# Optimization experiments

Hardware: AMD Instinct MI355X
Metric: run time of the kernel (lower is better)

Reference implementation:

```python
import jax, jax.numpy as jnp
import numpy as np

DIM = 1024; DEPTH = 2; HEADS = 8; DH = DIM // HEADS  # 128
BUCKET = 64; NHASH = 4; MULT = 4
B = 2; T = 4096
NBUCKETS = T // BUCKET  # 64
SCALE = DH ** -0.5
SELF_ATTN_VAL = -5e4  # TOKEN_SELF_ATTN_VALUE in reformer-pytorch
EPS = 1e-5


def layer_norm(x, g, b):
    m = jnp.mean(x, -1, keepdims=True)
    v = jnp.var(x, -1, keepdims=True)
    return (x - m) * jax.lax.rsqrt(v + EPS) * g + b


def lsh_attn(xn, Wqk, Wv, Wo, bo, rot):
    # xn: [B,T,DIM] already layer-normed. Shared-QK LSH attention (reformer-pytorch).
    qk = (xn @ Wqk).reshape(B, T, HEADS, DH).transpose(0, 2, 1, 3).reshape(B * HEADS, T, DH)
    v = (xn @ Wv).reshape(B, T, HEADS, DH).transpose(0, 2, 1, 3).reshape(B * HEADS, T, DH)
    bh = B * HEADS
    # --- hashing with random rotations ---
    rotated = jnp.einsum('btf,fhi->bhti', qk, rot)            # [bh,NHASH,T,NBUCKETS//2]
    rotated = jnp.concatenate([rotated, -rotated], -1)        # [bh,NHASH,T,NBUCKETS]
    buckets = jnp.argmax(rotated, -1)                         # [bh,NHASH,T]
    offs = (jnp.arange(NHASH) * NBUCKETS)[:, None]
    buckets = (buckets + offs).reshape(bh, NHASH * T)
    ticker = jnp.arange(NHASH * T)
    bt = buckets * T + (ticker % T)                           # unique keys -> stable-equivalent sort
    sticker = jnp.argsort(bt, axis=-1)                        # [bh, NHASH*T]
    undo = jnp.argsort(sticker, axis=-1)
    st = sticker % T                                          # original positions, bucket-sorted
    sqk = jnp.take_along_axis(qk, st[..., None], axis=1)
    sv = jnp.take_along_axis(v, st[..., None], axis=1)
    nchunks = NHASH * NBUCKETS
    bq_t = st.reshape(bh, nchunks, BUCKET)
    bqk = sqk.reshape(bh, nchunks, BUCKET, DH)
    bv = sv.reshape(bh, nchunks, BUCKET, DH)
    bq = bqk
    bk = bqk / jnp.clip(jnp.linalg.norm(bqk, axis=-1, keepdims=True), 1e-12)
    def look_one_back(a):
        extra = jnp.concatenate([a[:, -1:], a[:, :-1]], axis=1)
        return jnp.concatenate([a, extra], axis=2)
    bk = look_one_back(bk); bv = look_one_back(bv); bkv_t = look_one_back(bq_t)
    dots = jnp.einsum('bcie,bcje->bcij', bq, bk) * SCALE      # [bh,nchunks,BUCKET,2*BUCKET]
    self_mask = bq_t[..., :, None] == bkv_t[..., None, :]     # shared-QK: penalize i==j
    dots = jnp.where(self_mask, SELF_ATTN_VAL, dots)
    lse = jax.nn.logsumexp(dots, axis=-1, keepdims=True)
    p = jnp.exp(dots - lse)
    bo_ = jnp.einsum('bcij,bcje->bcie', p, bv)
    so = bo_.reshape(bh, NHASH * T, DH)
    slog = lse.reshape(bh, NHASH * T)
    o = jnp.take_along_axis(so, undo[..., None], axis=1)
    logits = jnp.take_along_axis(slog, undo, axis=1)
    o = o.reshape(bh, NHASH, T, DH)
    logits = logits.reshape(bh, NHASH, T, 1)
    probs = jnp.exp(logits - jax.nn.logsumexp(logits, axis=1, keepdims=True))
    out = jnp.sum(o * probs, axis=1)                          # combine hash rounds
    out = out.reshape(B, HEADS, T, DH).transpose(0, 2, 1, 3).reshape(B, T, HEADS * DH)
    return out @ Wo + bo


def setup_inputs() -> dict:
    key = jax.random.key(0)
    ks = jax.random.split(key, 16)
    s = 0.02
    d = {
        'x': jax.random.normal(ks[0], (B, T, DIM), jnp.float32),
        'ln1_g': jnp.ones((DEPTH, DIM), jnp.float32),
        'ln1_b': jnp.zeros((DEPTH, DIM), jnp.float32),
        'Wqk': jax.random.normal(ks[1], (DEPTH, DIM, HEADS * DH), jnp.float32) * s,
        'Wv': jax.random.normal(ks[2], (DEPTH, DIM, HEADS * DH), jnp.float32) * s,
        'Wo': jax.random.normal(ks[3], (DEPTH, HEADS * DH, DIM), jnp.float32) * s,
        'bo': jnp.zeros((DEPTH, DIM), jnp.float32),
        'ln2_g': jnp.ones((DEPTH, DIM), jnp.float32),
        'ln2_b': jnp.zeros((DEPTH, DIM), jnp.float32),
        'W1': jax.random.normal(ks[4], (DEPTH, DIM, DIM * MULT), jnp.float32) * s,
        'b1': jnp.zeros((DEPTH, DIM * MULT), jnp.float32),
        'W2': jax.random.normal(ks[5], (DEPTH, DIM * MULT, DIM), jnp.float32) * s,
        'b2': jnp.zeros((DEPTH, DIM), jnp.float32),
        'rotations': jax.random.normal(ks[6], (DEPTH, DH, NHASH, NBUCKETS // 2), jnp.float32),
    }
    return d


def reference(x, ln1_g, ln1_b, Wqk, Wv, Wo, bo, ln2_g, ln2_b, W1, b1, W2, b2, rotations):
    xx = jnp.concatenate([x, x], -1)  # [B,T,2*DIM] reversible pair
    def step(carry, p):
        g1, be1, wqk, wv, wo, bov, g2, be2, w1, bb1, w2, bb2, rot = p
        x1, x2 = jnp.split(carry, 2, axis=-1)
        y1 = x1 + lsh_attn(layer_norm(x2, g1, be1), wqk, wv, wo, bov, rot)
        h = layer_norm(y1, g2, be2)
        ff = jax.nn.gelu(h @ w1 + bb1, approximate=False) @ w2 + bb2
        y2 = x2 + ff
        return jnp.concatenate([y1, y2], -1), None
    params = (ln1_g, ln1_b, Wqk, Wv, Wo, bo, ln2_g, ln2_b, W1, b1, W2, b2, rotations)
    out, _ = jax.lax.scan(step, xx, params)
    y1, y2 = jnp.split(out, 2, axis=-1)
    return y1 + y2
```

## Files before the change

kernel.cpp:

```cpp
#include <hip/hip_runtime.h>
#include <hip/hip_bf16.h>
#include <cmath>

using bf16 = __hip_bfloat16;
typedef __attribute__((ext_vector_type(8))) short short8;
typedef __attribute__((ext_vector_type(4))) float floatx4;

__device__ __forceinline__ float bu2f(ushort u) { return __uint_as_float((unsigned)u << 16); }
__device__ __forceinline__ ushort f2bu(float f) {
  union { bf16 b; ushort u; } cv; cv.b = __float2bfloat16(f); return cv.u;
}
__device__ __forceinline__ void gl_lds16(const ushort* g, ushort* l) {
  __builtin_amdgcn_global_load_lds((const __attribute__((address_space(1))) unsigned*)g,
                                   (__attribute__((address_space(3))) unsigned*)l, 16, 0, 0);
}
__device__ __forceinline__ float fast_gelu(float x) {
  float z = 0.7978845608028654f * (x + 0.044715f * x * x * x);
  z = fmaxf(fminf(z, 10.f), -10.f);
  float e = __expf(2.f * z);
  float t = (e - 1.f) / (e + 1.f);
  return 0.5f * x * (1.f + t);
}

static constexpr int kT   = 4096;
static constexpr int kDim = 1024;
static constexpr float kScale   = 0.08838834764831845f;
static constexpr float kSelfVal = -5.0e4f;

__device__ __forceinline__ int sane_v(float f) { float a = fabsf(f); return (a > 1e-4f && a < 1e4f) ? 1 : 0; }

__global__ __launch_bounds__(256) void k_detect(const unsigned* __restrict__ x, int* __restrict__ flag) {
  __shared__ int cnt;
  int tid = threadIdx.x;
  if (tid == 0) cnt = 0;
  __syncthreads();
  int my = 0;
  const uint4* p = (const uint4*)x;
  for (int q = 0; q < 16; q++) {
    uint4 u = p[tid * 16 + q];
    my += sane_v(__uint_as_float(u.x << 16)) + sane_v(__uint_as_float(u.x & 0xffff0000u));
    my += sane_v(__uint_as_float(u.y << 16)) + sane_v(__uint_as_float(u.y & 0xffff0000u));
    my += sane_v(__uint_as_float(u.z << 16)) + sane_v(__uint_as_float(u.z & 0xffff0000u));
    my += sane_v(__uint_as_float(u.w << 16)) + sane_v(__uint_as_float(u.w & 0xffff0000u));
  }
  atomicAdd(&cnt, my);
  __syncthreads();
  if (tid == 0) flag[0] = (cnt >= 24576) ? 1 : 0;
}

__global__ __launch_bounds__(256) void k_cvt(const int* __restrict__ flag, const void* __restrict__ src,
                                             ushort* __restrict__ dst, int n) {
  int i = blockIdx.x * 256 + threadIdx.x;
  if (i >= n) return;
  dst[i] = (*flag) ? ((const ushort*)src)[i] : f2bu(((const float*)src)[i]);
}

__global__ __launch_bounds__(256) void k_init_any(const int* __restrict__ flag, const void* __restrict__ x,
                                                  float* __restrict__ x1, float* __restrict__ x2) {
  int i = blockIdx.x * 1024 + threadIdx.x * 4;
  float4 f;
  if (*flag) {
    ushort4 u = *(const ushort4*)((const ushort*)x + i);
    f.x = bu2f(u.x); f.y = bu2f(u.y); f.z = bu2f(u.z); f.w = bu2f(u.w);
  } else {
    f = *(const float4*)((const float*)x + i);
  }
  *(float4*)(x1 + i) = f;
  *(float4*)(x2 + i) = f;
}

__global__ __launch_bounds__(256) void k_final_any(const int* __restrict__ flag, const float* __restrict__ x1,
                                                   const float* __restrict__ x2, void* __restrict__ out) {
  int i = blockIdx.x * 1024 + threadIdx.x * 4;
  float4 a = *(const float4*)(x1 + i);
  float4 b = *(const float4*)(x2 + i);
  float4 s; s.x = a.x + b.x; s.y = a.y + b.y; s.z = a.z + b.z; s.w = a.w + b.w;
  if (*flag) {
    ushort4 u; u.x = f2bu(s.x); u.y = f2bu(s.y); u.z = f2bu(s.z); u.w = f2bu(s.w);
    *(ushort4*)((ushort*)out + i) = u;
  } else {
    *(float4*)((float*)out + i) = s;
  }
}

__global__ __launch_bounds__(256) void k_ln(const float* __restrict__ x, const ushort* __restrict__ g,
                                            const ushort* __restrict__ be, ushort* __restrict__ out) {
  __shared__ float ws[4], ws2[4];
  int row = blockIdx.x, tid = threadIdx.x;
  const float* xr = x + (size_t)row * kDim + tid * 4;
  float4 v = *(const float4*)xr;
  float s  = v.x + v.y + v.z + v.w;
  float s2 = v.x*v.x + v.y*v.y + v.z*v.z + v.w*v.w;
  #pragma unroll
  for (int off = 32; off; off >>= 1) { s += __shfl_down(s, off); s2 += __shfl_down(s2, off); }
  int wave = tid >> 6, lane = tid & 63;
  if (lane == 0) { ws[wave] = s; ws2[wave] = s2; }
  __syncthreads();
  s  = ws[0] + ws[1] + ws[2] + ws[3];
  s2 = ws2[0] + ws2[1] + ws2[2] + ws2[3];
  float mean = s * (1.f/1024.f);
  float var  = fmaxf(s2 * (1.f/1024.f) - mean*mean, 0.f);
  float rstd = rsqrtf(var + 1e-5f);
  int cb = tid * 4;
  ushort* o = out + (size_t)row * kDim + cb;
  o[0] = f2bu((v.x - mean) * rstd * bu2f(g[cb+0]) + bu2f(be[cb+0]));
  o[1] = f2bu((v.y - mean) * rstd * bu2f(g[cb+1]) + bu2f(be[cb+1]));
  o[2] = f2bu((v.z - mean) * rstd * bu2f(g[cb+2]) + bu2f(be[cb+2]));
  o[3] = f2bu((v.w - mean) * rstd * bu2f(g[cb+3]) + bu2f(be[cb+3]));
}

__global__ __launch_bounds__(256) void k_transpose2(const int* __restrict__ flag, const void* __restrict__ src_bf,
                                                    const void* __restrict__ src_f, ushort* __restrict__ out,
                                                    int K, int N) {
  __shared__ ushort tile[32][33];
  int isbf = *flag;
  int nb = blockIdx.x * 32, kb = blockIdx.y * 32;
  int tx = threadIdx.x & 31, ty = threadIdx.x >> 5;
  for (int r = ty; r < 32; r += 8) {
    size_t idx = (size_t)(kb + r) * N + nb + tx;
    tile[r][tx] = isbf ? ((const ushort*)src_bf)[idx] : f2bu(((const float*)src_f)[idx]);
  }
  __syncthreads();
  for (int r = ty; r < 32; r += 8) out[(size_t)(nb + r) * K + kb + tx] = tile[tx][r];
}

__global__ __launch_bounds__(256) void k_rot_t(const ushort* __restrict__ rot, ushort* __restrict__ rotT) {
  int tid = threadIdx.x;
  for (int idx = tid; idx < 16384; idx += 256) {
    int n = idx >> 7, k = idx & 127;
    rotT[idx] = rot[k * 128 + n];
  }
}

__global__ __launch_bounds__(256) void k_gemm(const ushort* __restrict__ A, const ushort* __restrict__ Bt,
                                              const ushort* __restrict__ bias, float* __restrict__ Cf,
                                              ushort* __restrict__ Cb, ushort* __restrict__ Cb2,
                                              int M, int N, int K, int mode) {
  __shared__ alignas(16) ushort As[128*64];
  __shared__ alignas(16) ushort Bs[128*64];
  const int tid = threadIdx.x;
  const int lane = tid & 63, wave = tid >> 6;
  const int m0 = blockIdx.y * 128, n0 = blockIdx.x * 128;
  const int wm = (wave & 1) * 64, wn = (wave >> 1) * 64;
  const int lr = lane & 15, lk = (lane >> 4) * 8;
  const int r8  = tid >> 3;
  const int cst = ((tid & 7) * 8) ^ ((r8 & 7) * 8);
  const int swz = (lr & 7) * 8;

  floatx4 acc[4][4];
  #pragma unroll
  for (int mi = 0; mi < 4; mi++)
    #pragma unroll
    for (int ni = 0; ni < 4; ni++) acc[mi][ni] = (floatx4){0.f, 0.f, 0.f, 0.f};

  const ushort* Ap = A  + (size_t)(m0 + r8) * K + cst;
  const ushort* Bp = Bt + (size_t)(n0 + r8) * K + cst;
  const size_t rstep = (size_t)32 * K;

  for (int k0 = 0; k0 < K; k0 += 64) {
    __syncthreads();
    #pragma unroll
    for (int i = 0; i < 4; i++) {
      gl_lds16(Ap + i * rstep + k0, As + i*2048 + wave*512);
      gl_lds16(Bp + i * rstep + k0, Bs + i*2048 + wave*512);
    }
    __syncthreads();
    #pragma unroll
    for (int ks = 0; ks < 2; ks++) {
      const int col = (ks*32 + lk) ^ swz;
      short8 a[4], b[4];
      #pragma unroll
      for (int mi = 0; mi < 4; mi++) a[mi] = *(const short8*)&As[(wm + mi*16 + lr)*64 + col];
      #pragma unroll
      for (int ni = 0; ni < 4; ni++) b[ni] = *(const short8*)&Bs[(wn + ni*16 + lr)*64 + col];
      #pragma unroll
      for (int mi = 0; mi < 4; mi++)
        #pragma unroll
        for (int ni = 0; ni < 4; ni++)
          acc[mi][ni] = __builtin_amdgcn_mfma_f32_16x16x32_bf16(a[mi], b[ni], acc[mi][ni], 0, 0, 0);
    }
  }
  #pragma unroll
  for (int mi = 0; mi < 4; mi++) {
    #pragma unroll
    for (int ni = 0; ni < 4; ni++) {
      int col = n0 + wn + ni*16 + lr;
      float bv = (mode == 1 || mode == 2) ? bu2f(bias[col]) : 0.f;
      #pragma unroll
      for (int q = 0; q < 4; q++) {
        int r2 = m0 + wm + mi*16 + (lane >> 4)*4 + q;
        float val = acc[mi][ni][q];
        if (mode == 0) {
          Cf[(size_t)r2 * N + col] = val;
        } else if (mode == 1) {
          Cf[(size_t)r2 * N + col] += val + bv;
        } else if (mode == 2) {
          Cb[(size_t)r2 * N + col] = f2bu(fast_gelu(val + bv));
        } else if (mode == 3) {
          Cb[(size_t)r2 * N + col] = f2bu(val);
        } else {
          ushort h = f2bu(val);
          Cb [(size_t)r2 * N + col] = h;
          Cb2[(size_t)r2 * N + col] = f2bu(val - bu2f(h));
        }
      }
    }
  }
}

__global__ __launch_bounds__(256) void k_bucket_mfma(const ushort* __restrict__ qkh, const ushort* __restrict__ qkl,
                                                     const ushort* __restrict__ rotT, int* __restrict__ bkt) {
  __shared__ alignas(16) ushort Bs[128*128];
  __shared__ alignas(16) ushort Ah[64*128];
  __shared__ alignas(16) ushort Al[64*128];
  const int tid = threadIdx.x;
  const int lane = tid & 63, wave = tid >> 6;
  const int lr = lane & 15, lk = (lane >> 4) * 8;
  const int tt = blockIdx.x * 64;
  const int bh = blockIdx.y;
  const int b = bh >> 3, hh = bh & 7;

  {
    int r = tid >> 2, c0 = (tid & 3) * 32;
    size_t base = ((size_t)(b * kT + tt + r)) * kDim + hh * 128 + c0;
    const uint4* sh = (const uint4*)(qkh + base);
    const uint4* sl = (const uint4*)(qkl + base);
    uint4* dh = (uint4*)&Ah[r * 128 + c0];
    uint4* dl = (uint4*)&Al[r * 128 + c0];
    #pragma unroll
    for (int i = 0; i < 4; i++) { dh[i] = sh[i]; dl[i] = sl[i]; }
  }
  {
    const uint4* src = (const uint4*)rotT;
    uint4* dst = (uint4*)Bs;
    for (int i = tid; i < 2048; i += 256) dst[i] = src[i];
  }
  __syncthreads();

  floatx4 acc[4][2];
  #pragma unroll
  for (int mi = 0; mi < 4; mi++) { acc[mi][0] = (floatx4){0,0,0,0}; acc[mi][1] = (floatx4){0,0,0,0}; }
  #pragma unroll
  for (int ks = 0; ks < 4; ks++) {
    short8 a[4], bb[2];
    #pragma unroll
    for (int ni = 0; ni < 2; ni++) bb[ni] = *(const short8*)&Bs[(wave*32 + ni*16 + lr)*128 + ks*32 + lk];
    #pragma unroll
    for (int mi = 0; mi < 4; mi++) a[mi] = *(const short8*)&Ah[(mi*16 + lr)*128 + ks*32 + lk];
    #pragma unroll
    for (int mi = 0; mi < 4; mi++)
      #pragma unroll
      for (int ni = 0; ni < 2; ni++)
        acc[mi][ni] = __builtin_amdgcn_mfma_f32_16x16x32_bf16(a[mi], bb[ni], acc[mi][ni], 0, 0, 0);
  }
  #pragma unroll
  for (int ks = 0; ks < 4; ks++) {
    short8 a[4], bb[2];
    #pragma unroll
    for (int ni = 0; ni < 2; ni++) bb[ni] = *(const short8*)&Bs[(wave*32 + ni*16 + lr)*128 + ks*32 + lk];
    #pragma unroll
    for (int mi = 0; mi < 4; mi++) a[mi] = *(const short8*)&Al[(mi*16 + lr)*128 + ks*32 + lk];
    #pragma unroll
    for (int mi = 0; mi < 4; mi++)
      #pragma unroll
      for (int ni = 0; ni < 2; ni++)
        acc[mi][ni] = __builtin_amdgcn_mfma_f32_16x16x32_bf16(a[mi], bb[ni], acc[mi][ni], 0, 0, 0);
  }

  #pragma unroll
  for (int mi = 0; mi < 4; mi++) {
    #pragma unroll
    for (int q = 0; q < 4; q++) {
      float v0 = acc[mi][0][q];
      float v1 = acc[mi][1][q];
      float best = v0; int bidx = lr;
      if (v1  > best) { best = v1;  bidx = 16 + lr; }
      if (-v0 > best) { best = -v0; bidx = 32 + lr; }
      if (-v1 > best) { best = -v1; bidx = 48 + lr; }
      #pragma unroll
      for (int m = 1; m <= 8; m <<= 1) {
        float ov = __shfl_xor(best, m);
        int   oi = __shfl_xor(bidx, m);
        if (ov > best || (ov == best && oi < bidx)) { best = ov; bidx = oi; }
      }
      if (lr == 0) {
        int row = mi*16 + ((lane >> 4) & 3)*4 + q;
        bkt[(bh*4 + wave)*4096 + tt + row] = bidx;
      }
    }
  }
}

__global__ __launch_bounds__(256) void k_sort(const int* __restrict__ bkt, int* __restrict__ st) {
  __shared__ unsigned char  hist[64*256];
  __shared__ unsigned short offs[64*256];
  __shared__ int base[64];
  int tid = threadIdx.x, grp = blockIdx.x;
  const int* bk = bkt + grp * 4096;
  for (int i = tid; i < 64*256; i += 256) hist[i] = 0;
  __syncthreads();
  int myb[16];
  #pragma unroll
  for (int j = 0; j < 16; j++) {
    myb[j] = bk[tid*16 + j];
    hist[myb[j]*256 + tid] += 1;
  }
  __syncthreads();
  if (tid < 64) {
    int run = 0;
    for (int t = 0; t < 256; t++) { offs[tid*256 + t] = (unsigned short)run; run += hist[tid*256 + t]; }
    base[tid] = run;
  }
  __syncthreads();
  if (tid == 0) {
    int run = 0;
    for (int b2 = 0; b2 < 64; b2++) { int c = base[b2]; base[b2] = run; run += c; }
  }
  __syncthreads();
  #pragma unroll
  for (int j = 0; j < 16; j++) {
    int b2 = myb[j];
    int r = 0;
    for (int jj = 0; jj < j; jj++) r += (myb[jj] == b2) ? 1 : 0;
    st[grp*4096 + base[b2] + (int)offs[b2*256 + tid] + r] = tid*16 + j;
  }
}

__global__ __launch_bounds__(256) void k_attn(const ushort* __restrict__ qkh, const ushort* __restrict__ vbuf,
                                              const int* __restrict__ st, ushort* __restrict__ o_r,
                                              float* __restrict__ lse_r) {
  __shared__ alignas(16) ushort KV[128*136];
  __shared__ alignas(16) ushort Ps[64*136];
  __shared__ float rnorm[128];
  __shared__ int   kposs[128];
  __shared__ float red1[64*4];
  __shared__ float red2[64*4];
  __shared__ float lrow[64];

  const int tid = threadIdx.x;
  const int bid = blockIdx.x;
  const int bh = bid >> 8;
  const int c  = bid & 255;
  const int h  = c >> 6;
  const int cprev = (c + 255) & 255;
  const int b  = bh >> 3, hh = bh & 7;
  const int lane = tid & 63, wave = tid >> 6;
  const int lr = lane & 15, lk = (lane >> 4) * 8;

  {
    int j = tid >> 1, half = tid & 1;
    int slot = (j < 64) ? (c*64 + j) : (cprev*64 + (j - 64));
    int pos = st[bh*16384 + slot];
    if (half == 0) kposs[j] = pos;
    const ushort* src = qkh + ((size_t)(b * kT + pos)) * kDim + hh*128 + half*64;
    float ss = 0.f;
    #pragma unroll
    for (int i2 = 0; i2 < 64; i2 += 8) {
      uint4 u = *(const uint4*)(src + i2);
      *(uint4*)&KV[j*136 + half*64 + i2] = u;
      float f0 = bu2f((ushort)(u.x & 0xffffu)), f1 = bu2f((ushort)(u.x >> 16));
      float f2 = bu2f((ushort)(u.y & 0xffffu)), f3 = bu2f((ushort)(u.y >> 16));
      float f4 = bu2f((ushort)(u.z & 0xffffu)), f5 = bu2f((ushort)(u.z >> 16));
      float f6 = bu2f((ushort)(u.w & 0xffffu)), f7 = bu2f((ushort)(u.w >> 16));
      ss += f0*f0 + f1*f1 + f2*f2 + f3*f3 + f4*f4 + f5*f5 + f6*f6 + f7*f7;
    }
    ss += __shfl_xor(ss, 1);
    if (half == 0) rnorm[j] = 1.f / fmaxf(sqrtf(ss), 1e-12f);
  }
  __syncthreads();

  {
    floatx4 acc[4][2];
    #pragma unroll
    for (int mi = 0; mi < 4; mi++) { acc[mi][0] = (floatx4){0,0,0,0}; acc[mi][1] = (floatx4){0,0,0,0}; }
    #pragma unroll
    for (int ks = 0; ks < 4; ks++) {
      short8 a[4], bb[2];
      #pragma unroll
      for (int mi = 0; mi < 4; mi++) a[mi]  = *(const short8*)&KV[(mi*16 + lr)*136 + ks*32 + lk];
      #pragma unroll
      for (int ni = 0; ni < 2; ni++) bb[ni] = *(const short8*)&KV[(wave*32 + ni*16 + lr)*136 + ks*32 + lk];
      #pragma unroll
      for (int mi = 0; mi < 4; mi++)
        #pragma unroll
        for (int ni = 0; ni < 2; ni++)
          acc[mi][ni] = __builtin_amdgcn_mfma_f32_16x16x32_bf16(a[mi], bb[ni], acc[mi][ni], 0, 0, 0);
    }
    #pragma unroll
    for (int mi = 0; mi < 4; mi++) {
      #pragma unroll
      for (int ni = 0; ni < 2; ni++) {
        int col = wave*32 + ni*16 + lr;
        float rn = rnorm[col] * kScale;
        int cpos = kposs[col];
        #pragma unroll
        for (int q = 0; q < 4; q++) {
          int row = mi*16 + (lane >> 4)*4 + q;
          float val = acc[mi][ni][q] * rn;
          if (cpos == kposs[row]) val = kSelfVal;
          Ps[row*136 + col] = f2bu(val);
        }
      }
    }
  }
  __syncthreads();

  {
    int j = tid >> 1, half = tid & 1;
    int pos = kposs[j];
    const ushort* src = vbuf + ((size_t)(b * kT + pos)) * kDim + hh*128 + half*64;
    #pragma unroll
    for (int i2 = 0; i2 < 64; i2 += 8) {
      uint4 u = *(const uint4*)(src + i2);
      int d0 = half*64 + i2;
      KV[(d0+0)*136 + j] = (ushort)(u.x & 0xffffu); KV[(d0+1)*136 + j] = (ushort)(u.x >> 16);
      KV[(d0+2)*136 + j] = (ushort)(u.y & 0xffffu); KV[(d0+3)*136 + j] = (ushort)(u.y >> 16);
      KV[(d0+4)*136 + j] = (ushort)(u.z & 0xffffu); KV[(d0+5)*136 + j] = (ushort)(u.z >> 16);
      KV[(d0+6)*136 + j] = (ushort)(u.w & 0xffffu); KV[(d0+7)*136 + j] = (ushort)(u.w >> 16);
    }
  }

  {
    int i = tid >> 2, part = tid & 3;
    const int jb = part * 32;
    float m = -1e30f;
    for (int j2 = 0; j2 < 32; j2++) m = fmaxf(m, bu2f(Ps[i*136 + jb + j2]));
    red1[i*4 + part] = m;
    __syncthreads();
    m = fmaxf(fmaxf(red1[i*4+0], red1[i*4+1]), fmaxf(red1[i*4+2], red1[i*4+3]));
    float ssum = 0.f;
    for (int j2 = 0; j2 < 32; j2++) {
      float arg = fmaxf(fminf(bu2f(Ps[i*136 + jb + j2]) - m, 0.f), -80.f);
      float p = __expf(arg);
      ssum += p;
      Ps[i*136 + jb + j2] = f2bu(p);
    }
    red2[i*4 + part] = ssum;
    __syncthreads();
    if (part == 0) {
      float l = fmaxf(red2[i*4+0] + red2[i*4+1] + red2[i*4+2] + red2[i*4+3], 1e-20f);
      lrow[i] = 1.f / l;
      lse_r[(size_t)(bh*4 + h)*4096 + kposs[i]] = m + __logf(l);
    }
  }
  __syncthreads();

  {
    floatx4 acc[4][2];
    #pragma unroll
    for (int mi = 0; mi < 4; mi++) { acc[mi][0] = (floatx4){0,0,0,0}; acc[mi][1] = (floatx4){0,0,0,0}; }
    #pragma unroll
    for (int ks = 0; ks < 4; ks++) {
      short8 a[4], bb[2];
      #pragma unroll
      for (int mi = 0; mi < 4; mi++) a[mi]  = *(const short8*)&Ps[(mi*16 + lr)*136 + ks*32 + lk];
      #pragma unroll
      for (int ni = 0; ni < 2; ni++) bb[ni] = *(const short8*)&KV[(wave*32 + ni*16 + lr)*136 + ks*32 + lk];
      #pragma unroll
      for (int mi = 0; mi < 4; mi++)
        #pragma unroll
        for (int ni = 0; ni < 2; ni++)
          acc[mi][ni] = __builtin_amdgcn_mfma_f32_16x16x32_bf16(a[mi], bb[ni], acc[mi][ni], 0, 0, 0);
    }
    #pragma unroll
    for (int mi = 0; mi < 4; mi++) {
      #pragma unroll
      for (int ni = 0; ni < 2; ni++) {
        int d = wave*32 + ni*16 + lr;
        #pragma unroll
        for (int q = 0; q < 4; q++) {
          int row = mi*16 + (lane >> 4)*4 + q;
          float o = acc[mi][ni][q] * lrow[row];
          o_r[((size_t)(bh*4 + h)*4096 + kposs[row])*128 + d] = f2bu(o);
        }
      }
    }
  }
}

__global__ __launch_bounds__(256) void k_combine(const ushort* __restrict__ o_r, const float* __restrict__ lse_r,
                                                 ushort* __restrict__ attnbf) {
  int rid = blockIdx.x * 2 + (threadIdx.x >> 7);
  int d = threadIdx.x & 127;
  int bh = rid >> 12, t = rid & 4095;
  int b = bh >> 3, hh = bh & 7;
  size_t base = (size_t)bh * 16384 + t;
  float l0 = lse_r[base], l1 = lse_r[base + 4096], l2 = lse_r[base + 8192], l3 = lse_r[base + 12288];
  float M = fmaxf(fmaxf(l0, l1), fmaxf(l2, l3));
  float e0 = __expf(fmaxf(fminf(l0 - M, 0.f), -80.f));
  float e1 = __expf(fmaxf(fminf(l1 - M, 0.f), -80.f));
  float e2 = __expf(fmaxf(fminf(l2 - M, 0.f), -80.f));
  float e3 = __expf(fmaxf(fminf(l3 - M, 0.f), -80.f));
  float inv = 1.f / (e0 + e1 + e2 + e3);
  float o = e0 * bu2f(o_r[(base         )*128 + d]) + e1 * bu2f(o_r[(base +  4096)*128 + d])
          + e2 * bu2f(o_r[(base +  8192)*128 + d]) + e3 * bu2f(o_r[(base + 12288)*128 + d]);
  attnbf[((size_t)b * kT + t) * kDim + hh*128 + d] = f2bu(o * inv);
}

extern "C" void kernel_launch(void* const* d_in, const int* in_sizes, int n_in,
                              void* d_out, int out_size, void* d_ws, size_t ws_size,
                              hipStream_t stream) {
  (void)in_sizes; (void)n_in; (void)out_size; (void)ws_size;
  const void* x     = d_in[0];
  const void* ln1_g = d_in[1];
  const void* ln1_b = d_in[2];
  const void* Wqk   = d_in[3];
  const void* Wv    = d_in[4];
  const void* Wo    = d_in[5];
  const void* bo    = d_in[6];
  const void* ln2_g = d_in[7];
  const void* ln2_b = d_in[8];
  const void* W1    = d_in[9];
  const void* b1    = d_in[10];
  const void* W2    = d_in[11];
  const void* b2    = d_in[12];
  const void* rot   = d_in[13];

  char* w = (char*)d_ws;
  int*    flag = (int*)w;    w += 256;
  ushort* prm  = (ushort*)w; w += 131072;
  float* x1  = (float*)w;  w += 33554432;
  float* x2  = (float*)w;  w += 33554432;
  ushort* qkh = (ushort*)w; w += 16777216;
  ushort* qkl = (ushort*)w; w += 16777216;
  ushort* vbb = (ushort*)w; w += 16777216;
  ushort* xbf = (ushort*)w; w += 16777216;
  ushort* orb = (ushort*)w; w += 67108864;
  float* lse = (float*)w;  w += 1048576;
  int*   bkt = (int*)w;    w += 1048576;
  int*   stb = (int*)w;    w += 1048576;
  ushort* wtA = (ushort*)w; w += 2097152;
  ushort* wtB = (ushort*)w; w += 2097152;
  ushort* wtC = (ushort*)w; w += 2097152;
  ushort* wt1 = (ushort*)w; w += 8388608;
  ushort* wt2 = (ushort*)w; w += 8388608;
  ushort* rtT = (ushort*)w; w += 32768;

  ushort* pLN1G = prm + 0;     ushort* pLN1B = prm + 2048;
  ushort* pBO   = prm + 4096;  ushort* pLN2G = prm + 6144;
  ushort* pLN2B = prm + 8192;  ushort* pB1   = prm + 10240;
  ushort* pB2   = prm + 18432; ushort* pROT  = prm + 20480;

  k_detect<<<1, 256, 0, stream>>>((const unsigned*)x, flag);
  k_cvt<<<8,   256, 0, stream>>>(flag, ln1_g, pLN1G, 2048);
  k_cvt<<<8,   256, 0, stream>>>(flag, ln1_b, pLN1B, 2048);
  k_cvt<<<8,   256, 0, stream>>>(flag, bo,    pBO,   2048);
  k_cvt<<<8,   256, 0, stream>>>(flag, ln2_g, pLN2G, 2048);
  k_cvt<<<8,   256, 0, stream>>>(flag, ln2_b, pLN2B, 2048);
  k_cvt<<<32,  256, 0, stream>>>(flag, b1,    pB1,   8192);
  k_cvt<<<8,   256, 0, stream>>>(flag, b2,    pB2,   2048);
  k_cvt<<<128, 256, 0, stream>>>(flag, rot,   pROT,  32768);
  k_init_any<<<8192, 256, 0, stream>>>(flag, x, x1, x2);

  for (int d = 0; d < 2; d++) {
    k_transpose2<<<dim3(32, 32),  256, 0, stream>>>(flag,
        (const char*)Wqk + (size_t)d*1048576*2, (const char*)Wqk + (size_t)d*1048576*4, wtA, 1024, 1024);
    k_transpose2<<<dim3(32, 32),  256, 0, stream>>>(flag,
        (const char*)Wv  + (size_t)d*1048576*2, (const char*)Wv  + (size_t)d*1048576*4, wtB, 1024, 1024);
    k_transpose2<<<dim3(32, 32),  256, 0, stream>>>(flag,
        (const char*)Wo  + (size_t)d*1048576*2, (const char*)Wo  + (size_t)d*1048576*4, wtC, 1024, 1024);
    k_transpose2<<<dim3(128, 32), 256, 0, stream>>>(flag,
        (const char*)W1  + (size_t)d*4194304*2, (const char*)W1  + (size_t)d*4194304*4, wt1, 1024, 4096);
    k_transpose2<<<dim3(32, 128), 256, 0, stream>>>(flag,
        (const char*)W2  + (size_t)d*4194304*2, (const char*)W2  + (size_t)d*4194304*4, wt2, 4096, 1024);
    k_rot_t<<<1, 256, 0, stream>>>(pROT + (size_t)d * 16384, rtT);

    k_ln<<<8192, 256, 0, stream>>>(x2, pLN1G + d*1024, pLN1B + d*1024, xbf);
    k_gemm<<<dim3(8, 64), 256, 0, stream>>>(xbf, wtA, nullptr, nullptr, qkh, qkl, 8192, 1024, 1024, 5);
    k_gemm<<<dim3(8, 64), 256, 0, stream>>>(xbf, wtB, nullptr, nullptr, vbb, nullptr, 8192, 1024, 1024, 3);
    k_bucket_mfma<<<dim3(64, 16), 256, 0, stream>>>(qkh, qkl, rtT, bkt);
    k_sort<<<64, 256, 0, stream>>>(bkt, stb);
    k_attn<<<4096, 256, 0, stream>>>(qkh, vbb, stb, orb, lse);
    k_combine<<<32768, 256, 0, stream>>>(orb, lse, xbf);
    k_gemm<<<dim3(8, 64), 256, 0, stream>>>(xbf, wtC, pBO + d*1024, x1, nullptr, nullptr, 8192, 1024, 1024, 1);
    k_ln<<<8192, 256, 0, stream>>>(x1, pLN2G + d*1024, pLN2B + d*1024, xbf);
    k_gemm<<<dim3(32, 64), 256, 0, stream>>>(xbf, wt1, pB1 + d*4096, nullptr, orb, nullptr, 8192, 4096, 1024, 2);
    k_gemm<<<dim3(8, 64), 256, 0, stream>>>(orb, wt2, pB2 + d*1024, x2, nullptr, nullptr, 8192, 1024, 4096, 1);
  }
  k_final_any<<<8192, 256, 0, stream>>>(flag, x1, x2, d_out);
}
```

Before: 1.267 ms.

## Replace GEMM with 4-stage pipelined 512-thread kernel and block swizzle

Replaces the single-buffered 128x128 GEMM with a templated kernel that uses 256-wide N tiles, 512 threads, and a 4-deep ring of LDS buffers filled by async global-to-LDS loads with explicit vmcnt waits. It also remaps block ids for L2 locality and raises MFMA priority with setprio. The goal is to overlap global loads with MFMA work and raise arithmetic intensity for the dense projections and FFN GEMMs. In exchange it uses more LDS, which lowers occupancy, and the hand-counted waitcnt values must match the number of outstanding loads.

```diff
diff --git a/kernel.cpp b/kernel.cpp
--- a/kernel.cpp
+++ b/kernel.cpp
@@ -132,67 +132,119 @@
   }
 }
 
-__global__ __launch_bounds__(256) void k_gemm(const ushort* __restrict__ A, const ushort* __restrict__ Bt,
-                                              const ushort* __restrict__ bias, float* __restrict__ Cf,
-                                              ushort* __restrict__ Cb, ushort* __restrict__ Cb2,
-                                              int M, int N, int K, int mode) {
-  __shared__ alignas(16) ushort As[128*64];
-  __shared__ alignas(16) ushort Bs[128*64];
-  const int tid = threadIdx.x;
+template <int MW>
+__global__ __launch_bounds__(512, 2) void k_gemm2(const ushort* __restrict__ A, const ushort* __restrict__ Bt,
+                                                  const ushort* __restrict__ bias, float* __restrict__ Cf,
+                                                  ushort* __restrict__ Cb, ushort* __restrict__ Cb2,
+                                                  int M, int N, int K, int mode) {
+  constexpr int BM  = MW * 32;
+  constexpr int LA  = MW / 4;
+  __shared__ alignas(16) ushort SA[4][BM * 32];
+  __shared__ alignas(16) ushort SB[4][256 * 32];
+
+  const int tid  = threadIdx.x;
   const int lane = tid & 63, wave = tid >> 6;
-  const int m0 = blockIdx.y * 128, n0 = blockIdx.x * 128;
-  const int wm = (wave & 1) * 64, wn = (wave >> 1) * 64;
-  const int lr = lane & 15, lk = (lane >> 4) * 8;
-  const int r8  = tid >> 3;
-  const int cst = ((tid & 7) * 8) ^ ((r8 & 7) * 8);
-  const int swz = (lr & 7) * 8;
-
-  floatx4 acc[4][4];
-  #pragma unroll
-  for (int mi = 0; mi < 4; mi++)
+  const int lr = lane & 15, g = lane >> 4;
+  const int wm = wave >> 2, wn = wave & 3;
+
+  const int nbx = gridDim.x;
+  const int nwg = nbx * gridDim.y;
+  const int bid = blockIdx.y * nbx + blockIdx.x;
+  const int swz = (bid & 7) * (nwg >> 3) + (bid >> 3);
+  const int m0 = (swz / nbx) * BM;
+  const int n0 = (swz % nbx) * 256;
+
+  const int NT = K >> 5;
+
+  const ushort* srcA[LA];
+  #pragma unroll
+  for (int j = 0; j < LA; j++) {
+    int chunk = wave * (64 * LA) + j * 64 + lane;
+    int row = chunk >> 2, c = chunk & 3;
+    int cs = c ^ ((row >> 1) & 3);
+    srcA[j] = A + (size_t)(m0 + row) * K + cs * 8;
+  }
+  const ushort* srcB[2];
+  #pragma unroll
+  for (int j = 0; j < 2; j++) {
+    int chunk = wave * 128 + j * 64 + lane;
+    int row = chunk >> 2, c = chunk & 3;
+    int cs = c ^ ((row >> 1) & 3);
+    srcB[j] = Bt + (size_t)(n0 + row) * K + cs * 8;
+  }
+
+  int offA[MW], offB[4];
+  #pragma unroll
+  for (int mi = 0; mi < MW; mi++) {
+    int row = wm * (MW * 16) + mi * 16 + lr;
+    offA[mi] = row * 32 + ((g ^ ((row >> 1) & 3)) * 8);
+  }
+  #pragma unroll
+  for (int ni = 0; ni < 4; ni++) {
+    int row = wn * 64 + ni * 16 + lr;
+    offB[ni] = row * 32 + ((g ^ ((row >> 1) & 3)) * 8);
+  }
+
+  floatx4 acc[MW][4];
+  #pragma unroll
+  for (int mi = 0; mi < MW; mi++)
     #pragma unroll
     for (int ni = 0; ni < 4; ni++) acc[mi][ni] = (floatx4){0.f, 0.f, 0.f, 0.f};
 
-  const ushort* Ap = A  + (size_t)(m0 + r8) * K + cst;
-  const ushort* Bp = Bt + (size_t)(n0 + r8) * K + cst;
-  const size_t rstep = (size_t)32 * K;
-
-  for (int k0 = 0; k0 < K; k0 += 64) {
-    __syncthreads();
-    #pragma unroll
-    for (int i = 0; i < 4; i++) {
-      gl_lds16(Ap + i * rstep + k0, As + i*2048 + wave*512);
-      gl_lds16(Bp + i * rstep + k0, Bs + i*2048 + wave*512);
-    }
-    __syncthreads();
-    #pragma unroll
-    for (int ks = 0; ks < 2; ks++) {
-      const int col = (ks*32 + lk) ^ swz;
-      short8 a[4], b[4];
-      #pragma unroll
-      for (int mi = 0; mi < 4; mi++) a[mi] = *(const short8*)&As[(wm + mi*16 + lr)*64 + col];
-      #pragma unroll
-      for (int ni = 0; ni < 4; ni++) b[ni] = *(const short8*)&Bs[(wn + ni*16 + lr)*64 + col];
-      #pragma unroll
-      for (int mi = 0; mi < 4; mi++)
-        #pragma unroll
-        for (int ni = 0; ni < 4; ni++)
-          acc[mi][ni] = __builtin_amdgcn_mfma_f32_16x16x32_bf16(a[mi], b[ni], acc[mi][ni], 0, 0, 0);
-    }
-  }
-  #pragma unroll
-  for (int mi = 0; mi < 4; mi++) {
+  #pragma unroll
+  for (int p = 0; p < 3; p++) {
+    #pragma unroll
+    for (int j = 0; j < LA; j++) gl_lds16(srcA[j] + p * 32, &SA[p][(wave * (64 * LA) + j * 64) * 8]);
+    #pragma unroll
+    for (int j = 0; j < 2; j++)  gl_lds16(srcB[j] + p * 32, &SB[p][(wave * 128 + j * 64) * 8]);
+  }
+
+  for (int t = 0; t < NT; t++) {
+    asm volatile("" ::: "memory");
+    if (t + 3 < NT) {
+      const int kp = (t + 3) * 32, pb = (t + 3) & 3;
+      #pragma unroll
+      for (int j = 0; j < LA; j++) gl_lds16(srcA[j] + kp, &SA[pb][(wave * (64 * LA) + j * 64) * 8]);
+      #pragma unroll
+      for (int j = 0; j < 2; j++)  gl_lds16(srcB[j] + kp, &SB[pb][(wave * 128 + j * 64) * 8]);
+      if constexpr (MW == 8) asm volatile("s_waitcnt vmcnt(12)" ::: "memory");
+      else                   asm volatile("s_waitcnt vmcnt(9)"  ::: "memory");
+    } else {
+      asm volatile("s_waitcnt vmcnt(0)" ::: "memory");
+    }
+    __builtin_amdgcn_s_barrier();
+    __builtin_amdgcn_sched_barrier(0);
+
+    const ushort* sa = SA[t & 3];
+    const ushort* sb = SB[t & 3];
+    short8 a[MW], b[4];
+    #pragma unroll
+    for (int mi = 0; mi < MW; mi++) a[mi] = *(const short8*)&sa[offA[mi]];
+    #pragma unroll
+    for (int ni = 0; ni < 4; ni++)  b[ni] = *(const short8*)&sb[offB[ni]];
+    __builtin_amdgcn_s_setprio(1);
+    #pragma unroll
+    for (int mi = 0; mi < MW; mi++)
+      #pragma unroll
+      for (int ni = 0; ni < 4; ni++)
+        acc[mi][ni] = __builtin_amdgcn_mfma_f32_16x16x32_bf16(a[mi], b[ni], acc[mi][ni], 0, 0, 0);
+    __builtin_amdgcn_s_setprio(0);
+
+    __builtin_amdgcn_sched_barrier(0);
+    __builtin_amdgcn_s_barrier();
+  }
+
+  #pragma unroll
+  for (int mi = 0; mi < MW; mi++) {
     #pragma unroll
     for (int ni = 0; ni < 4; ni++) {
-      int col = n0 + wn + ni*16 + lr;
+      int col = n0 + wn * 64 + ni * 16 + lr;
       float bv = (mode == 1 || mode == 2) ? bu2f(bias[col]) : 0.f;
       #pragma unroll
       for (int q = 0; q < 4; q++) {
-        int r2 = m0 + wm + mi*16 + (lane >> 4)*4 + q;
+        int r2 = m0 + wm * (MW * 16) + mi * 16 + (lane >> 4) * 4 + q;
         float val = acc[mi][ni][q];
-        if (mode == 0) {
-          Cf[(size_t)r2 * N + col] = val;
-        } else if (mode == 1) {
+        if (mode == 1) {
           Cf[(size_t)r2 * N + col] += val + bv;
         } else if (mode == 2) {
           Cb[(size_t)r2 * N + col] = f2bu(fast_gelu(val + bv));
@@ -206,6 +258,7 @@
       }
     }
   }
+  (void)M;
 }
 
 __global__ __launch_bounds__(256) void k_bucket_mfma(const ushort* __restrict__ qkh, const ushort* __restrict__ qkl,
@@ -566,16 +619,16 @@
     k_rot_t<<<1, 256, 0, stream>>>(pROT + (size_t)d * 16384, rtT);
 
     k_ln<<<8192, 256, 0, stream>>>(x2, pLN1G + d*1024, pLN1B + d*1024, xbf);
-    k_gemm<<<dim3(8, 64), 256, 0, stream>>>(xbf, wtA, nullptr, nullptr, qkh, qkl, 8192, 1024, 1024, 5);
-    k_gemm<<<dim3(8, 64), 256, 0, stream>>>(xbf, wtB, nullptr, nullptr, vbb, nullptr, 8192, 1024, 1024, 3);
+    k_gemm2<4><<<dim3(4, 64), 512, 0, stream>>>(xbf, wtA, nullptr, nullptr, qkh, qkl, 8192, 1024, 1024, 5);
+    k_gemm2<4><<<dim3(4, 64), 512, 0, stream>>>(xbf, wtB, nullptr, nullptr, vbb, nullptr, 8192, 1024, 1024, 3);
     k_bucket_mfma<<<dim3(64, 16), 256, 0, stream>>>(qkh, qkl, rtT, bkt);
     k_sort<<<64, 256, 0, stream>>>(bkt, stb);
     k_attn<<<4096, 256, 0, stream>>>(qkh, vbb, stb, orb, lse);
     k_combine<<<32768, 256, 0, stream>>>(orb, lse, xbf);
-    k_gemm<<<dim3(8, 64), 256, 0, stream>>>(xbf, wtC, pBO + d*1024, x1, nullptr, nullptr, 8192, 1024, 1024, 1);
+    k_gemm2<4><<<dim3(4, 64), 512, 0, stream>>>(xbf, wtC, pBO + d*1024, x1, nullptr, nullptr, 8192, 1024, 1024, 1);
     k_ln<<<8192, 256, 0, stream>>>(x1, pLN2G + d*1024, pLN2B + d*1024, xbf);
-    k_gemm<<<dim3(32, 64), 256, 0, stream>>>(xbf, wt1, pB1 + d*4096, nullptr, orb, nullptr, 8192, 4096, 1024, 2);
-    k_gemm<<<dim3(8, 64), 256, 0, stream>>>(orb, wt2, pB2 + d*1024, x2, nullptr, nullptr, 8192, 1024, 4096, 1);
+    k_gemm2<8><<<dim3(16, 32), 512, 0, stream>>>(xbf, wt1, pB1 + d*4096, nullptr, orb, nullptr, 8192, 4096, 1024, 2);
+    k_gemm2<4><<<dim3(4, 64), 512, 0, stream>>>(orb, wt2, pB2 + d*1024, x2, nullptr, nullptr, 8192, 1024, 4096, 1);
   }
   k_final_any<<<8192, 256, 0, stream>>>(flag, x1, x2, d_out);
 }
```

Result: slower. 1.555 ms (+22.8%).
